# Kernel optimization log

Measured on AMD Instinct MI355X. Metric: run time of the kernel, lower is better.

The kernel has to match this reference:

```python
import jax, jax.numpy as jnp
import numpy as np

N_NODES = 50000
N_EDGES = 800000
C_IN = 64
C_OUT = 64
K = 3


def setup_inputs() -> dict:
    key = jax.random.key(0)
    k1, k2, k3, k4, k5, k6 = jax.random.split(key, 6)
    x = jax.random.normal(k1, (N_NODES, C_IN), dtype=jnp.float32)
    edge_index = jax.random.randint(k2, (2, N_EDGES), 0, N_NODES, dtype=jnp.int32)
    edge_weight = jax.random.uniform(k3, (N_EDGES,), dtype=jnp.float32)
    # Xavier-uniform init for [K, C_IN, C_OUT] (fan over last two dims)
    limit = float(np.sqrt(6.0 / (C_IN + C_OUT)))
    theta_forward = jax.random.uniform(k4, (K, C_IN, C_OUT), minval=-limit, maxval=limit, dtype=jnp.float32)
    theta_backward = jax.random.uniform(k5, (K, C_IN, C_OUT), minval=-limit, maxval=limit, dtype=jnp.float32)
    return {
        "x": x,
        "edge_index": edge_index,
        "edge_weight": edge_weight,
        "theta_forward": theta_forward,
        "theta_backward": theta_backward,
    }


def _propagate(x, row, col, edge_weight, n_nodes):
    # degree normalization: deg[i] = sum of edge_weight over edges with row == i
    deg = jax.ops.segment_sum(edge_weight, row, num_segments=n_nodes)
    deg_inv = jnp.where(deg > 0, jax.lax.rsqrt(jnp.where(deg > 0, deg, 1.0)), 0.0)
    norm = deg_inv[row] * edge_weight * deg_inv[col]      # [E]
    msg = norm[:, None] * x[col]                          # [E, C] gather-scale
    return jax.ops.segment_sum(msg, row, num_segments=n_nodes)  # scatter-add -> [N, C]


def reference(x, edge_index, edge_weight, theta_forward, theta_backward):
    row, col = edge_index[0], edge_index[1]
    n_nodes = x.shape[0]
    k = theta_forward.shape[0]
    Tx_0 = x
    Tx_1 = _propagate(x, row, col, edge_weight, n_nodes)
    out = Tx_0 @ theta_forward[0] + Tx_1 @ theta_backward[0]
    for i in range(1, k):
        Tx_2 = _propagate(Tx_1, row, col, edge_weight, n_nodes)
        out = out + Tx_2 @ theta_forward[i] + Tx_1 @ theta_backward[i]
        Tx_1 = Tx_2
    return out
```

## Files before the change

kernel.cpp:

```cpp
#include <hip/hip_runtime.h>
#include <hip/hip_fp16.h>


#define N_NODES 50000
#define N_EDGES 800000
#define C 64
#define CAP 64
#define NPART 196
#define CAPP 4608
#define EPB 2048
#define NEB 391
#define XH_BLOCKS 782
#define CW_BLOCKS 16

typedef _Float16 half8 __attribute__((ext_vector_type(8)));
typedef float f32x4 __attribute__((ext_vector_type(4)));

__global__ __launch_bounds__(1024) void scatter2_kernel(
        const int* __restrict__ row, const int* __restrict__ col,
        const float* __restrict__ w, int* __restrict__ percur,
        uint2* __restrict__ pedges,
        const float* __restrict__ x, __half* __restrict__ xh,
        const float* __restrict__ tf, const float* __restrict__ tb,
        _Float16* __restrict__ whc) {
    const int tid = threadIdx.x;
    if (blockIdx.x >= NEB + XH_BLOCKS) {
        int idx = (blockIdx.x - NEB - XH_BLOCKS) * 1024 + tid;
        int j = idx >> 12;
        int rem = idx & 4095;
        int ci = rem >> 6;
        int co = rem & 63;
        float v;
        if (j == 0)      v = tf[rem];
        else if (j == 1) v = tb[rem] + tb[4096 + rem];
        else if (j == 2) v = tf[4096 + rem] + tb[8192 + rem];
        else             v = tf[8192 + rem];
        whc[(j << 12) + (co << 6) + ci] = (_Float16)v;
        return;
    }
    if (blockIdx.x >= NEB) {
        int i = (blockIdx.x - NEB) * 1024 + tid;
        if (i < N_NODES * C / 4) {
            float4 v = ((const float4*)x)[i];
            union { float2 f2; __half2 h2[2]; } u;
            u.h2[0] = __floats2half2_rn(v.x, v.y);
            u.h2[1] = __floats2half2_rn(v.z, v.w);
            ((float2*)xh)[i] = u.f2;
        }
        return;
    }
    __shared__ int h[NPART];
    __shared__ int cur[NPART];
    uint2 ent[2];
    int pp[2];
    if (tid < NPART) h[tid] = 0;
    __syncthreads();
    int base = blockIdx.x * EPB;
#pragma unroll
    for (int i = 0; i < 2; ++i) {
        int e = base + i * 1024 + tid;
        pp[i] = -1;
        if (e < N_EDGES) {
            int r = row[e];
            unsigned int c = (unsigned int)col[e];
            unsigned int wh = (unsigned int)__half_as_ushort(__float2half_rn(w[e]));
            ent[i] = make_uint2((c << 16) | wh, (unsigned int)(r & 255));
            pp[i] = r >> 8;
            atomicAdd(&h[pp[i]], 1);
        }
    }
    __syncthreads();
    if (tid < NPART) cur[tid] = atomicAdd(&percur[tid], h[tid]);
    __syncthreads();
#pragma unroll
    for (int i = 0; i < 2; ++i) {
        if (pp[i] >= 0) {
            int slot = atomicAdd(&cur[pp[i]], 1);
            pedges[(size_t)pp[i] * CAPP + slot] = ent[i];
        }
    }
}

__global__ __launch_bounds__(1024) void build_kernel(
        const uint2* __restrict__ pedges, const int* __restrict__ percur,
        unsigned int* __restrict__ bkt, int* __restrict__ cnt,
        float* __restrict__ dinv) {
    __shared__ unsigned int lbuck[256 * CAP];
    __shared__ int lcnt[256];
    const int tid = threadIdx.x;
    const int p = blockIdx.x;
    if (tid < 256) lcnt[tid] = 0;
    __syncthreads();
    int e = min(percur[p], CAPP);
    const uint2* src = pedges + (size_t)p * CAPP;
    for (int i = tid; i < e; i += 1024) {
        uint2 en = src[i];
        int rl = (int)en.y;
        int slot = atomicAdd(&lcnt[rl], 1);
        if (slot < CAP) lbuck[(rl << 6) + slot] = en.x;
    }
    __syncthreads();
    if (tid < 256) {
        int m = min(lcnt[tid], CAP);
        int g = (p << 8) + tid;
        float sum = 0.f;
        for (int j = 0; j < m; ++j)
            sum += __half2float(__ushort_as_half(
                (unsigned short)(lbuck[(tid << 6) + j] & 0xFFFFu)));
        if (g < N_NODES) {
            cnt[g] = m;
            dinv[g] = (sum > 0.f) ? rsqrtf(sum) : 0.f;
        }
    }
    __syncthreads();
    const uint4* s4 = (const uint4*)lbuck;
    uint4* dst = (uint4*)(bkt + ((size_t)p << 14));
    for (int i = tid; i < 256 * CAP / 4; i += 1024) dst[i] = s4[i];
}

template <bool FIXW, bool FUSE_GEMM>
__global__ __launch_bounds__(256) void prop_kernel(
        const __half* __restrict__ xin, __half* __restrict__ xout,
        const int* __restrict__ cnt, unsigned int* __restrict__ bkt,
        const float* __restrict__ dinv,
        const __half* __restrict__ x0, const __half* __restrict__ x1,
        const _Float16* __restrict__ whc, float* __restrict__ out) {
    const int tid = threadIdx.x;
    const int wib = tid >> 6;
    const int lane = tid & 63;
    const int q = lane >> 4;
    const int ql = lane & 15;
    const int node = (blockIdx.x << 4) + (wib << 2) + q;
    int m = min(cnt[node], CAP);
    int base = node << 6;
    int cj[4];
    float nj[4];
#pragma unroll
    for (int s = 0; s < 4; ++s) {
        int idx = (s << 4) + ql;
        cj[s] = 0;
        nj[s] = 0.f;
        if (idx < m) {
            unsigned int b = bkt[base + idx];
            int c = (int)(b >> 16);
            cj[s] = c << 6;
            float wv = __half2float(__ushort_as_half((unsigned short)(b & 0xFFFFu)));
            if constexpr (FIXW) {
                float nn = wv * dinv[c];
                nj[s] = nn;
                bkt[base + idx] = ((unsigned int)c << 16) |
                    (unsigned int)__half_as_ushort(__float2half_rn(nn));
            } else {
                nj[s] = wv;
            }
        }
    }
    float ax = 0.f, ay = 0.f, az = 0.f, aw = 0.f;
#pragma unroll
    for (int s = 0; s < 4; ++s) {
        int cb = s << 4;
        if (cb >= m) break;
        int rem = m - cb;
        if (rem > 16) rem = 16;
        int mm = (rem + 7) & ~7;
        for (int jo = 0; jo < mm; jo += 8) {
            int cs[8];
            float ns[8];
            float2 vs[8];
#pragma unroll
            for (int t = 0; t < 8; ++t) {
                cs[t] = __shfl(cj[s], (q << 4) + jo + t);
                ns[t] = __shfl(nj[s], (q << 4) + jo + t);
            }
#pragma unroll
            for (int t = 0; t < 8; ++t)
                vs[t] = *(const float2*)(xin + cs[t] + (ql << 2));
#pragma unroll
            for (int t = 0; t < 8; ++t) {
                const __half2* hp = (const __half2*)&vs[t];
                float2 a = __half22float2(hp[0]);
                float2 b = __half22float2(hp[1]);
                ax += ns[t] * a.x;
                ay += ns[t] * a.y;
                az += ns[t] * b.x;
                aw += ns[t] * b.y;
            }
        }
    }
    float dr = dinv[node];
    union { float2 f2; __half2 h2[2]; } u;
    u.h2[0] = __floats2half2_rn(dr * ax, dr * ay);
    u.h2[1] = __floats2half2_rn(dr * az, dr * aw);
    if constexpr (!FUSE_GEMM) {
        *(float2*)(xout + ((size_t)node << 6) + (ql << 2)) = u.f2;
    } else {
        __shared__ _Float16 tcl[16 * 72];
        *(float2*)(void*)&tcl[((wib << 2) + q) * 72 + (ql << 2)] = u.f2;
        __syncthreads();
        const int mbase = blockIdx.x << 4;
        const __half* gsrc[3] = {x0, x1, xin};
        const size_t abase = ((size_t)(mbase + ql) << 6) + (q << 3);
        f32x4 acc = {};
#pragma unroll
        for (int j = 0; j < 4; ++j) {
#pragma unroll
            for (int kk = 0; kk < 64; kk += 32) {
                half8 af;
                if (j < 3)
                    af = *(const half8*)(const void*)(gsrc[j] + abase + kk);
                else
                    af = *(const half8*)(const void*)&tcl[ql * 72 + (q << 3) + kk];
                const _Float16* wb = whc + (j << 12) + (((wib << 4) + ql) << 6)
                                         + (q << 3) + kk;
                half8 bf = *(const half8*)(const void*)wb;
                acc = __builtin_amdgcn_mfma_f32_16x16x32_f16(af, bf, acc, 0, 0, 0);
            }
        }
#pragma unroll
        for (int i = 0; i < 4; ++i) {
            int r = mbase + (q << 2) + i;
            out[((size_t)r << 6) + (wib << 4) + ql] = acc[i];
        }
    }
}

extern "C" void kernel_launch(void* const* d_in, const int* in_sizes, int n_in,
                              void* d_out, int out_size, void* d_ws, size_t ws_size,
                              hipStream_t stream) {
    const float* x  = (const float*)d_in[0];
    const int*   ei = (const int*)d_in[1];
    const float* ew = (const float*)d_in[2];
    const float* tf = (const float*)d_in[3];
    const float* tb = (const float*)d_in[4];
    float* out = (float*)d_out;

    const int* row = ei;
    const int* col = ei + N_EDGES;

    const int NROWS_PAD = NPART * 256;
    float* ws = (float*)d_ws;
    size_t off = 0;
    int*    percur = (int*)(ws + off); off += 256;
    uint2*  pedges = (uint2*)(ws + off); off += (size_t)NPART * CAPP * 2;
    unsigned int* bkt = (unsigned int*)(ws + off); off += (size_t)NROWS_PAD * CAP;
    int*    cnt  = (int*)(ws + off); off += NROWS_PAD;
    float*  dinv = ws + off; off += NROWS_PAD;
    __half* xh   = (__half*)(ws + off); off += (size_t)N_NODES * C / 2;
    __half* tA   = (__half*)(ws + off); off += (size_t)N_NODES * C / 2;
    __half* tB   = (__half*)(ws + off); off += (size_t)N_NODES * C / 2;
    __half* tC   = (__half*)(ws + off); off += (size_t)N_NODES * C / 2;
    _Float16* whc = (_Float16*)(ws + off); off += 4 * 64 * 64 / 2;

    hipMemsetAsync(percur, 0, NPART * sizeof(int), stream);

    scatter2_kernel<<<NEB + XH_BLOCKS + CW_BLOCKS, 1024, 0, stream>>>(
        row, col, ew, percur, pedges, x, xh, tf, tb, whc);
    build_kernel<<<NPART, 1024, 0, stream>>>(pedges, percur, bkt, cnt, dinv);

    const int PB = N_NODES / 16;
    prop_kernel<true,  false><<<PB, 256, 0, stream>>>(
        xh, tA, cnt, bkt, dinv, nullptr, nullptr, nullptr, nullptr);
    prop_kernel<false, false><<<PB, 256, 0, stream>>>(
        tA, tB, cnt, bkt, dinv, nullptr, nullptr, nullptr, nullptr);
    prop_kernel<false, true><<<PB, 256, 0, stream>>>(
        tB, tC, cnt, bkt, dinv, xh, tA, whc, out);
}
```

Measured before the change: 162.4 us.

## Replace two-pass partitioned bucketing with direct global-atomic row buckets

```diff
diff --git a/kernel.cpp b/kernel.cpp
--- a/kernel.cpp
+++ b/kernel.cpp
@@ -6,26 +6,23 @@
 #define N_EDGES 800000
 #define C 64
 #define CAP 64
-#define NPART 196
-#define CAPP 4608
-#define EPB 2048
-#define NEB 391
+#define EB 196
 #define XH_BLOCKS 782
 #define CW_BLOCKS 16
 
 typedef _Float16 half8 __attribute__((ext_vector_type(8)));
 typedef float f32x4 __attribute__((ext_vector_type(4)));
 
-__global__ __launch_bounds__(1024) void scatter2_kernel(
+__global__ __launch_bounds__(1024) void scatter_kernel(
         const int* __restrict__ row, const int* __restrict__ col,
-        const float* __restrict__ w, int* __restrict__ percur,
-        uint2* __restrict__ pedges,
+        const float* __restrict__ w, int* __restrict__ cnt,
+        unsigned int* __restrict__ bkt,
         const float* __restrict__ x, __half* __restrict__ xh,
         const float* __restrict__ tf, const float* __restrict__ tb,
         _Float16* __restrict__ whc) {
     const int tid = threadIdx.x;
-    if (blockIdx.x >= NEB + XH_BLOCKS) {
-        int idx = (blockIdx.x - NEB - XH_BLOCKS) * 1024 + tid;
+    if (blockIdx.x >= EB + XH_BLOCKS) {
+        int idx = (blockIdx.x - EB - XH_BLOCKS) * 1024 + tid;
         int j = idx >> 12;
         int rem = idx & 4095;
         int ci = rem >> 6;
@@ -38,8 +35,8 @@
         whc[(j << 12) + (co << 6) + ci] = (_Float16)v;
         return;
     }
-    if (blockIdx.x >= NEB) {
-        int i = (blockIdx.x - NEB) * 1024 + tid;
+    if (blockIdx.x >= EB) {
+        int i = (blockIdx.x - EB) * 1024 + tid;
         if (i < N_NODES * C / 4) {
             float4 v = ((const float4*)x)[i];
             union { float2 f2; __half2 h2[2]; } u;
@@ -49,73 +46,50 @@
         }
         return;
     }
-    __shared__ int h[NPART];
-    __shared__ int cur[NPART];
-    uint2 ent[2];
-    int pp[2];
-    if (tid < NPART) h[tid] = 0;
-    __syncthreads();
-    int base = blockIdx.x * EPB;
-#pragma unroll
-    for (int i = 0; i < 2; ++i) {
-        int e = base + i * 1024 + tid;
-        pp[i] = -1;
-        if (e < N_EDGES) {
-            int r = row[e];
-            unsigned int c = (unsigned int)col[e];
-            unsigned int wh = (unsigned int)__half_as_ushort(__float2half_rn(w[e]));
-            ent[i] = make_uint2((c << 16) | wh, (unsigned int)(r & 255));
-            pp[i] = r >> 8;
-            atomicAdd(&h[pp[i]], 1);
-        }
-    }
-    __syncthreads();
-    if (tid < NPART) cur[tid] = atomicAdd(&percur[tid], h[tid]);
-    __syncthreads();
-#pragma unroll
-    for (int i = 0; i < 2; ++i) {
-        if (pp[i] >= 0) {
-            int slot = atomicAdd(&cur[pp[i]], 1);
-            pedges[(size_t)pp[i] * CAPP + slot] = ent[i];
-        }
-    }
-}
-
-__global__ __launch_bounds__(1024) void build_kernel(
-        const uint2* __restrict__ pedges, const int* __restrict__ percur,
-        unsigned int* __restrict__ bkt, int* __restrict__ cnt,
+    int e0 = (blockIdx.x * 1024 + tid) * 4;
+    if (e0 < N_EDGES) {
+        int4   r4 = *(const int4*)(row + e0);
+        int4   c4 = *(const int4*)(col + e0);
+        float4 w4 = *(const float4*)(w + e0);
+        int rr[4] = {r4.x, r4.y, r4.z, r4.w};
+        int cc[4] = {c4.x, c4.y, c4.z, c4.w};
+        float ww[4] = {w4.x, w4.y, w4.z, w4.w};
+#pragma unroll
+        for (int i = 0; i < 4; ++i) {
+            unsigned int wh =
+                (unsigned int)__half_as_ushort(__float2half_rn(ww[i]));
+            int slot = atomicAdd(&cnt[rr[i]], 1);
+            if (slot < CAP)
+                bkt[((size_t)rr[i] << 6) + slot] =
+                    ((unsigned int)cc[i] << 16) | wh;
+        }
+    }
+}
+
+__global__ __launch_bounds__(256) void dinv_kernel(
+        const int* __restrict__ cnt, const unsigned int* __restrict__ bkt,
         float* __restrict__ dinv) {
-    __shared__ unsigned int lbuck[256 * CAP];
-    __shared__ int lcnt[256];
     const int tid = threadIdx.x;
-    const int p = blockIdx.x;
-    if (tid < 256) lcnt[tid] = 0;
-    __syncthreads();
-    int e = min(percur[p], CAPP);
-    const uint2* src = pedges + (size_t)p * CAPP;
-    for (int i = tid; i < e; i += 1024) {
-        uint2 en = src[i];
-        int rl = (int)en.y;
-        int slot = atomicAdd(&lcnt[rl], 1);
-        if (slot < CAP) lbuck[(rl << 6) + slot] = en.x;
-    }
-    __syncthreads();
-    if (tid < 256) {
-        int m = min(lcnt[tid], CAP);
-        int g = (p << 8) + tid;
-        float sum = 0.f;
-        for (int j = 0; j < m; ++j)
+    const int wib = tid >> 6;
+    const int lane = tid & 63;
+    const int q = lane >> 4;
+    const int ql = lane & 15;
+    const int node = (blockIdx.x << 4) + (wib << 2) + q;
+    int m = min(cnt[node], CAP);
+    size_t base = (size_t)node << 6;
+    float sum = 0.f;
+#pragma unroll
+    for (int s = 0; s < 4; ++s) {
+        int idx = (s << 4) + ql;
+        if (idx < m)
             sum += __half2float(__ushort_as_half(
-                (unsigned short)(lbuck[(tid << 6) + j] & 0xFFFFu)));
-        if (g < N_NODES) {
-            cnt[g] = m;
-            dinv[g] = (sum > 0.f) ? rsqrtf(sum) : 0.f;
-        }
-    }
-    __syncthreads();
-    const uint4* s4 = (const uint4*)lbuck;
-    uint4* dst = (uint4*)(bkt + ((size_t)p << 14));
-    for (int i = tid; i < 256 * CAP / 4; i += 1024) dst[i] = s4[i];
+                (unsigned short)(bkt[base + idx] & 0xFFFFu)));
+    }
+    sum += __shfl_xor(sum, 1);
+    sum += __shfl_xor(sum, 2);
+    sum += __shfl_xor(sum, 4);
+    sum += __shfl_xor(sum, 8);
+    if (ql == 0) dinv[node] = (sum > 0.f) ? rsqrtf(sum) : 0.f;
 }
 
 template <bool FIXW, bool FUSE_GEMM>
@@ -237,27 +211,26 @@
     const int* row = ei;
     const int* col = ei + N_EDGES;
 
-    const int NROWS_PAD = NPART * 256;
+    const int NROWS_PAD = 50176;
     float* ws = (float*)d_ws;
     size_t off = 0;
-    int*    percur = (int*)(ws + off); off += 256;
-    uint2*  pedges = (uint2*)(ws + off); off += (size_t)NPART * CAPP * 2;
-    unsigned int* bkt = (unsigned int*)(ws + off); off += (size_t)NROWS_PAD * CAP;
     int*    cnt  = (int*)(ws + off); off += NROWS_PAD;
     float*  dinv = ws + off; off += NROWS_PAD;
+    unsigned int* bkt = (unsigned int*)(ws + off); off += (size_t)NROWS_PAD * CAP;
     __half* xh   = (__half*)(ws + off); off += (size_t)N_NODES * C / 2;
     __half* tA   = (__half*)(ws + off); off += (size_t)N_NODES * C / 2;
     __half* tB   = (__half*)(ws + off); off += (size_t)N_NODES * C / 2;
     __half* tC   = (__half*)(ws + off); off += (size_t)N_NODES * C / 2;
     _Float16* whc = (_Float16*)(ws + off); off += 4 * 64 * 64 / 2;
 
-    hipMemsetAsync(percur, 0, NPART * sizeof(int), stream);
-
-    scatter2_kernel<<<NEB + XH_BLOCKS + CW_BLOCKS, 1024, 0, stream>>>(
-        row, col, ew, percur, pedges, x, xh, tf, tb, whc);
-    build_kernel<<<NPART, 1024, 0, stream>>>(pedges, percur, bkt, cnt, dinv);
+    hipMemsetAsync(cnt, 0, NROWS_PAD * sizeof(int), stream);
+
+    scatter_kernel<<<EB + XH_BLOCKS + CW_BLOCKS, 1024, 0, stream>>>(
+        row, col, ew, cnt, bkt, x, xh, tf, tb, whc);
 
     const int PB = N_NODES / 16;
+    dinv_kernel<<<PB, 256, 0, stream>>>(cnt, bkt, dinv);
+
     prop_kernel<true,  false><<<PB, 256, 0, stream>>>(
         xh, tA, cnt, bkt, dinv, nullptr, nullptr, nullptr, nullptr);
     prop_kernel<false, false><<<PB, 256, 0, stream>>>(
```

New measurement: 186.4 us. 14.7% more time.
